# Kernel tuning notes

Hardware: AMD Instinct MI355X
Metric: run time of the kernel (lower is better)

Reference implementation:

```python
import jax, jax.numpy as jnp
import numpy as np

NUM_GRAPHS = 512

def setup_inputs() -> dict:
    key = jax.random.key(0)
    ks = jax.random.split(key, 16)
    N, E, F_IN, D = 50000, 800000, 128, 64
    x = jax.random.normal(ks[0], (N, F_IN), dtype=jnp.float32)
    edge_index = jax.random.randint(ks[1], (2, E), 0, N, dtype=jnp.int32)
    batch_index = jnp.sort(jax.random.randint(ks[2], (N,), 0, NUM_GRAPHS, dtype=jnp.int32))
    def lin(k, fin, fout):
        s = 1.0 / np.sqrt(fin)
        return jax.random.uniform(k, (fin, fout), jnp.float32, -s, s)
    return {
        "x": x, "edge_index": edge_index, "batch_index": batch_index,
        "W0": lin(ks[3], F_IN, D), "b0": jnp.zeros((D,), jnp.float32),
        "W1": lin(ks[4], D, D), "b1": jnp.zeros((D,), jnp.float32),
        "W2": lin(ks[5], D, D), "b2": jnp.zeros((D,), jnp.float32),
        "W3": lin(ks[6], D, D), "b3": jnp.zeros((D,), jnp.float32),
        "Wout": lin(ks[7], 2 * D, 1), "bout": jnp.zeros((1,), jnp.float32),
    }

def _gcn_edges(edge_index, N):
    # add self-loops and compute symmetric normalization D^-1/2 (A+I) D^-1/2
    loops = jnp.arange(N, dtype=edge_index.dtype)
    row = jnp.concatenate([edge_index[0], loops])  # source
    col = jnp.concatenate([edge_index[1], loops])  # target
    deg = jax.ops.segment_sum(jnp.ones_like(col, dtype=jnp.float32), col, num_segments=N)
    dinv = jnp.where(deg > 0, jax.lax.rsqrt(deg), 0.0)
    norm = dinv[row] * dinv[col]  # [E+N]
    return row, col, norm

def _gcn_conv(h, row, col, norm, W, b, N):
    h = h @ W                                   # [N, D] linear transform first
    msg = h[row] * norm[:, None]                # gather + scale
    out = jax.ops.segment_sum(msg, col, num_segments=N)  # scatter-add
    return out + b

def reference(x, edge_index, batch_index, W0, b0, W1, b1, W2, b2, W3, b3, Wout, bout):
    N = x.shape[0]
    row, col, norm = _gcn_edges(edge_index, N)
    h = jnp.tanh(_gcn_conv(x, row, col, norm, W0, b0, N))
    h = jnp.tanh(_gcn_conv(h, row, col, norm, W1, b1, N))
    h = jnp.tanh(_gcn_conv(h, row, col, norm, W2, b2, N))
    h = jnp.tanh(_gcn_conv(h, row, col, norm, W3, b3, N))
    gmax = jax.ops.segment_max(h, batch_index, num_segments=NUM_GRAPHS)
    gmax = jnp.where(jnp.isfinite(gmax), gmax, 0.0)  # empty segments -> 0
    gsum = jax.ops.segment_sum(h, batch_index, num_segments=NUM_GRAPHS)
    cnt = jax.ops.segment_sum(jnp.ones((N,), jnp.float32), batch_index, num_segments=NUM_GRAPHS)
    gmean = gsum / jnp.maximum(cnt, 1.0)[:, None]
    hidden = jnp.concatenate([gmax, gmean], axis=1)   # [G, 2D]
    out = hidden @ Wout + bout                        # [G, 1]
    return out, hidden
```

## Files before the change

kernel.cpp:

```cpp
#include <hip/hip_runtime.h>
#include <math.h>

#define CAP 64
typedef unsigned short ushort_t;
typedef unsigned int uint_t;

__global__ __launch_bounds__(256) void k_scatter2(const int* __restrict__ row,
                                                  const int* __restrict__ col, int E, int N,
                                                  int* __restrict__ deg, ushort_t* __restrict__ csr) {
    const int part = blockIdx.x & 7;
    const int slot = blockIdx.x >> 3;
    const int nslots = gridDim.x >> 3;
    const int lo = (int)((long long)N * part / 8);
    const int hi = (int)((long long)N * (part + 1) / 8);
    for (int e = slot * blockDim.x + threadIdx.x; e < E; e += nslots * blockDim.x) {
        int c = col[e];
        if (c >= lo && c < hi) {
            int d = atomicAdd(&deg[c], 1);
            if (d < CAP) csr[((size_t)c << 6) + d] = (ushort_t)row[e];
        }
    }
}

template <int K>
__global__ __launch_bounds__(256) void k_gemm(const float* __restrict__ X,
                                              const float* __restrict__ W,
                                              const int* __restrict__ deg,
                                              float* __restrict__ Gb, int N) {
    __shared__ __align__(16) float Wl[64 * 64];
    __shared__ __align__(16) float Xl[64 * 68];

    const int tid = threadIdx.x;
    const int wave = tid >> 6, lane = tid & 63;
    const int d8 = lane & 7, ns = lane >> 3;
    const int n0 = wave * 16 + ns, n1 = n0 + 8;

    const int base = blockIdx.x * 64;
    if (base >= N) return;
    const int tile_n = min(64, N - base);

    float4 a0l = {0,0,0,0}, a0h = {0,0,0,0}, a1l = {0,0,0,0}, a1h = {0,0,0,0};

    for (int kh = 0; kh < K / 64; kh++) {
        __syncthreads();
        for (int i = tid; i < 1024; i += 256)
            ((float4*)Wl)[i] = ((const float4*)(W + kh * 4096))[i];
        for (int idx = tid; idx < 1024; idx += 256) {
            int n = idx >> 4, q = idx & 15;
            float4 v = {0,0,0,0};
            if (n < tile_n) v = ((const float4*)(X + (size_t)(base + n) * K + kh * 64))[q];
            ((float4*)(Xl + n * 68))[q] = v;
        }
        __syncthreads();

        const float4* xq0 = (const float4*)(Xl + n0 * 68);
        const float4* xq1 = (const float4*)(Xl + n1 * 68);
        const float* wcol = Wl + d8 * 8;
#pragma unroll 2
        for (int kq = 0; kq < 16; kq++) {
            const float4 x4a = xq0[kq];
            const float4 x4b = xq1[kq];
            const float xs0[4] = {x4a.x, x4a.y, x4a.z, x4a.w};
            const float xs1[4] = {x4b.x, x4b.y, x4b.z, x4b.w};
#pragma unroll
            for (int j = 0; j < 4; j++) {
                const int k = kq * 4 + j;
                const float4 wa = *(const float4*)(wcol + k * 64);
                const float4 wb = *(const float4*)(wcol + k * 64 + 4);
                const float xa = xs0[j];
                const float xb = xs1[j];
                a0l.x = fmaf(xa, wa.x, a0l.x); a0l.y = fmaf(xa, wa.y, a0l.y);
                a0l.z = fmaf(xa, wa.z, a0l.z); a0l.w = fmaf(xa, wa.w, a0l.w);
                a0h.x = fmaf(xa, wb.x, a0h.x); a0h.y = fmaf(xa, wb.y, a0h.y);
                a0h.z = fmaf(xa, wb.z, a0h.z); a0h.w = fmaf(xa, wb.w, a0h.w);
                a1l.x = fmaf(xb, wa.x, a1l.x); a1l.y = fmaf(xb, wa.y, a1l.y);
                a1l.z = fmaf(xb, wa.z, a1l.z); a1l.w = fmaf(xb, wa.w, a1l.w);
                a1h.x = fmaf(xb, wb.x, a1h.x); a1h.y = fmaf(xb, wb.y, a1h.y);
                a1h.z = fmaf(xb, wb.z, a1h.z); a1h.w = fmaf(xb, wb.w, a1h.w);
            }
        }
    }

    int gn0 = base + n0, gn1 = base + n1;
    if (gn0 < N) {
        float s = rsqrtf((float)(deg[gn0] + 1));
        float4* ptr = (float4*)(Gb + (size_t)gn0 * 64);
        ptr[d8 * 2]     = make_float4(a0l.x * s, a0l.y * s, a0l.z * s, a0l.w * s);
        ptr[d8 * 2 + 1] = make_float4(a0h.x * s, a0h.y * s, a0h.z * s, a0h.w * s);
    }
    if (gn1 < N) {
        float s = rsqrtf((float)(deg[gn1] + 1));
        float4* ptr = (float4*)(Gb + (size_t)gn1 * 64);
        ptr[d8 * 2]     = make_float4(a1l.x * s, a1l.y * s, a1l.z * s, a1l.w * s);
        ptr[d8 * 2 + 1] = make_float4(a1h.x * s, a1h.y * s, a1h.z * s, a1h.w * s);
    }
}

__global__ __launch_bounds__(256) void k_agg(const float* __restrict__ Gb,
                                             const int* __restrict__ deg,
                                             const ushort_t* __restrict__ csr,
                                             const float* __restrict__ bias,
                                             float* __restrict__ H, int N) {
    int n = blockIdx.x * 4 + (threadIdx.x >> 6);
    if (n >= N) return;
    int lane = threadIdx.x & 63;
    int cnt = deg[n]; if (cnt > CAP) cnt = CAP;
    const ushort_t* rowp = csr + ((size_t)n << 6);
    float a0 = Gb[(size_t)n * 64 + lane];
    float a1 = 0.f, a2 = 0.f, a3 = 0.f, a4 = 0.f, a5 = 0.f, a6 = 0.f, a7 = 0.f;
    int i = 0;
    for (; i + 16 <= cnt; i += 16) {
        uint4 q0 = *(const uint4*)(rowp + i);
        uint4 q1 = *(const uint4*)(rowp + i + 8);
        int j0 = q0.x & 0xffff, j1 = q0.x >> 16, j2 = q0.y & 0xffff, j3 = q0.y >> 16;
        int j4 = q0.z & 0xffff, j5 = q0.z >> 16, j6 = q0.w & 0xffff, j7 = q0.w >> 16;
        int j8 = q1.x & 0xffff, j9 = q1.x >> 16, jA = q1.y & 0xffff, jB = q1.y >> 16;
        int jC = q1.z & 0xffff, jD = q1.z >> 16, jE = q1.w & 0xffff, jF = q1.w >> 16;
        float g0 = Gb[(size_t)j0 * 64 + lane], g1 = Gb[(size_t)j1 * 64 + lane];
        float g2 = Gb[(size_t)j2 * 64 + lane], g3 = Gb[(size_t)j3 * 64 + lane];
        float g4 = Gb[(size_t)j4 * 64 + lane], g5 = Gb[(size_t)j5 * 64 + lane];
        float g6 = Gb[(size_t)j6 * 64 + lane], g7 = Gb[(size_t)j7 * 64 + lane];
        float g8 = Gb[(size_t)j8 * 64 + lane], g9 = Gb[(size_t)j9 * 64 + lane];
        float gA = Gb[(size_t)jA * 64 + lane], gB = Gb[(size_t)jB * 64 + lane];
        float gC = Gb[(size_t)jC * 64 + lane], gD = Gb[(size_t)jD * 64 + lane];
        float gE = Gb[(size_t)jE * 64 + lane], gF = Gb[(size_t)jF * 64 + lane];
        a0 += g0; a1 += g1; a2 += g2; a3 += g3;
        a4 += g4; a5 += g5; a6 += g6; a7 += g7;
        a0 += g8; a1 += g9; a2 += gA; a3 += gB;
        a4 += gC; a5 += gD; a6 += gE; a7 += gF;
    }
    if (i + 8 <= cnt) {
        uint4 q = *(const uint4*)(rowp + i);
        int j0 = q.x & 0xffff, j1 = q.x >> 16, j2 = q.y & 0xffff, j3 = q.y >> 16;
        int j4 = q.z & 0xffff, j5 = q.z >> 16, j6 = q.w & 0xffff, j7 = q.w >> 16;
        a0 += Gb[(size_t)j0 * 64 + lane]; a1 += Gb[(size_t)j1 * 64 + lane];
        a2 += Gb[(size_t)j2 * 64 + lane]; a3 += Gb[(size_t)j3 * 64 + lane];
        a4 += Gb[(size_t)j4 * 64 + lane]; a5 += Gb[(size_t)j5 * 64 + lane];
        a6 += Gb[(size_t)j6 * 64 + lane]; a7 += Gb[(size_t)j7 * 64 + lane];
        i += 8;
    }
    if (i + 4 <= cnt) {
        uint2 q = *(const uint2*)(rowp + i);
        int j0 = q.x & 0xffff, j1 = q.x >> 16, j2 = q.y & 0xffff, j3 = q.y >> 16;
        a0 += Gb[(size_t)j0 * 64 + lane]; a1 += Gb[(size_t)j1 * 64 + lane];
        a2 += Gb[(size_t)j2 * 64 + lane]; a3 += Gb[(size_t)j3 * 64 + lane];
        i += 4;
    }
    if (i + 2 <= cnt) {
        uint_t q = *(const uint_t*)(rowp + i);
        a4 += Gb[(size_t)(q & 0xffff) * 64 + lane];
        a5 += Gb[(size_t)(q >> 16) * 64 + lane];
        i += 2;
    }
    if (i < cnt) a6 += Gb[(size_t)rowp[i] * 64 + lane];
    float acc = ((a0 + a1) + (a2 + a3)) + ((a4 + a5) + (a6 + a7));
    float dinv = rsqrtf((float)(cnt + 1));
    H[(size_t)n * 64 + lane] = tanhf(acc * dinv + bias[lane]);
}

__global__ __launch_bounds__(256) void k_pool(const float* __restrict__ H,
                                              const int* __restrict__ batch, int N, int Gn,
                                              const float* __restrict__ Wout,
                                              const float* __restrict__ bout,
                                              float* __restrict__ out,
                                              float* __restrict__ hidden) {
    int g = blockIdx.x * 4 + (threadIdx.x >> 6);
    if (g >= Gn) return;
    int lane = threadIdx.x & 63;
    int lo = 0, hi = N;
    while (lo < hi) { int m = (lo + hi) >> 1; if (batch[m] < g) lo = m + 1; else hi = m; }
    int s = lo;
    lo = s; hi = N;
    while (lo < hi) { int m = (lo + hi) >> 1; if (batch[m] < g + 1) lo = m + 1; else hi = m; }
    int c = lo - s;

    float m0 = -INFINITY, m1 = -INFINITY, m2 = -INFINITY, m3 = -INFINITY;
    float s0 = 0.f, s1 = 0.f, s2 = 0.f, s3 = 0.f;
    int n = s;
    for (; n + 3 < s + c; n += 4) {
        float v0 = H[(size_t)n * 64 + lane];
        float v1 = H[(size_t)(n + 1) * 64 + lane];
        float v2 = H[(size_t)(n + 2) * 64 + lane];
        float v3 = H[(size_t)(n + 3) * 64 + lane];
        m0 = fmaxf(m0, v0); s0 += v0;
        m1 = fmaxf(m1, v1); s1 += v1;
        m2 = fmaxf(m2, v2); s2 += v2;
        m3 = fmaxf(m3, v3); s3 += v3;
    }
    for (; n < s + c; n++) {
        float v = H[(size_t)n * 64 + lane];
        m0 = fmaxf(m0, v); s0 += v;
    }
    float vmax = fmaxf(fmaxf(m0, m1), fmaxf(m2, m3));
    float vsum = (s0 + s1) + (s2 + s3);
    float gmax = (c > 0) ? vmax : 0.f;
    float gmean = (c > 0) ? vsum / (float)c : 0.f;
    hidden[(size_t)g * 128 + lane] = gmax;
    hidden[(size_t)g * 128 + 64 + lane] = gmean;
    float p = fmaf(gmax, Wout[lane], gmean * Wout[64 + lane]);
    for (int o = 32; o > 0; o >>= 1) p += __shfl_down(p, o);
    if (lane == 0) out[g] = p + bout[0];
}

extern "C" void kernel_launch(void* const* d_in, const int* in_sizes, int n_in,
                              void* d_out, int out_size, void* d_ws, size_t ws_size,
                              hipStream_t stream) {
    const float* x    = (const float*)d_in[0];
    const int*   ei   = (const int*)d_in[1];
    const int*   batch= (const int*)d_in[2];
    const float* W0 = (const float*)d_in[3];  const float* b0 = (const float*)d_in[4];
    const float* W1 = (const float*)d_in[5];  const float* b1 = (const float*)d_in[6];
    const float* W2 = (const float*)d_in[7];  const float* b2 = (const float*)d_in[8];
    const float* W3 = (const float*)d_in[9];  const float* b3 = (const float*)d_in[10];
    const float* Wout = (const float*)d_in[11]; const float* bout = (const float*)d_in[12];

    const int N  = in_sizes[2];
    const int E  = in_sizes[1] / 2;
    const int Gn = out_size / 129;

    const int* row = ei;
    const int* col = ei + E;

    float* out_p    = (float*)d_out;
    float* hidden_p = out_p + Gn;

    char* wp = (char*)d_ws;
    auto alloc = [&](size_t bytes) { void* p = (void*)wp; wp += (bytes + 255) & ~(size_t)255; return p; };
    int*      deg  = (int*)alloc((size_t)N * 4);
    ushort_t* csr  = (ushort_t*)alloc((size_t)N * CAP * 2);
    float*    Gbuf = (float*)alloc((size_t)N * 64 * 4);
    float*    Ha   = (float*)alloc((size_t)N * 64 * 4);
    float*    Hb   = (float*)alloc((size_t)N * 64 * 4);

    hipMemsetAsync(deg, 0, (size_t)N * 4, stream);
    k_scatter2<<<2048, 256, 0, stream>>>(row, col, E, N, deg, csr);

    const int gblocks = (N + 63) / 64;
    const int ablocks = (N + 3) / 4;

    k_gemm<128><<<gblocks, 256, 0, stream>>>(x, W0, deg, Gbuf, N);
    k_agg<<<ablocks, 256, 0, stream>>>(Gbuf, deg, csr, b0, Ha, N);
    k_gemm<64><<<gblocks, 256, 0, stream>>>(Ha, W1, deg, Gbuf, N);
    k_agg<<<ablocks, 256, 0, stream>>>(Gbuf, deg, csr, b1, Hb, N);
    k_gemm<64><<<gblocks, 256, 0, stream>>>(Hb, W2, deg, Gbuf, N);
    k_agg<<<ablocks, 256, 0, stream>>>(Gbuf, deg, csr, b2, Ha, N);
    k_gemm<64><<<gblocks, 256, 0, stream>>>(Ha, W3, deg, Gbuf, N);
    k_agg<<<ablocks, 256, 0, stream>>>(Gbuf, deg, csr, b3, Hb, N);

    k_pool<<<(Gn + 3) / 4, 256, 0, stream>>>(Hb, batch, N, Gn, Wout, bout, out_p, hidden_p);
}
```

Measured before the change: 330.8 us.

## Fuse aggregation with next layer GEMM and final aggregation with pooling

Each layer's neighbor aggregation plus tanh now feeds directly into the next layer's 64x64 transform through shared memory, so each intermediate H is never written to or re-read from global memory. The last aggregation is merged into the graph pooling kernel, one block per graph, and the launch count falls from ten to six. The trade-offs are that each fused block runs the gather for 64 nodes serially per wave, 16 each, before its GEMM, and the pooling kernel gives only four waves to each graph's roughly 100 nodes. This could hurt latency hiding and load balance.

```diff
diff --git a/kernel.cpp b/kernel.cpp
--- a/kernel.cpp
+++ b/kernel.cpp
@@ -20,6 +20,59 @@
             if (d < CAP) csr[((size_t)c << 6) + d] = (ushort_t)row[e];
         }
     }
+}
+
+__device__ __forceinline__ float agg_gather(const float* __restrict__ Gb,
+                                            const ushort_t* __restrict__ rowp,
+                                            int cnt, int self, int lane) {
+    float a0 = Gb[(size_t)self * 64 + lane];
+    float a1 = 0.f, a2 = 0.f, a3 = 0.f, a4 = 0.f, a5 = 0.f, a6 = 0.f, a7 = 0.f;
+    int i = 0;
+    for (; i + 16 <= cnt; i += 16) {
+        uint4 q0 = *(const uint4*)(rowp + i);
+        uint4 q1 = *(const uint4*)(rowp + i + 8);
+        int j0 = q0.x & 0xffff, j1 = q0.x >> 16, j2 = q0.y & 0xffff, j3 = q0.y >> 16;
+        int j4 = q0.z & 0xffff, j5 = q0.z >> 16, j6 = q0.w & 0xffff, j7 = q0.w >> 16;
+        int j8 = q1.x & 0xffff, j9 = q1.x >> 16, jA = q1.y & 0xffff, jB = q1.y >> 16;
+        int jC = q1.z & 0xffff, jD = q1.z >> 16, jE = q1.w & 0xffff, jF = q1.w >> 16;
+        float g0 = Gb[(size_t)j0 * 64 + lane], g1 = Gb[(size_t)j1 * 64 + lane];
+        float g2 = Gb[(size_t)j2 * 64 + lane], g3 = Gb[(size_t)j3 * 64 + lane];
+        float g4 = Gb[(size_t)j4 * 64 + lane], g5 = Gb[(size_t)j5 * 64 + lane];
+        float g6 = Gb[(size_t)j6 * 64 + lane], g7 = Gb[(size_t)j7 * 64 + lane];
+        float g8 = Gb[(size_t)j8 * 64 + lane], g9 = Gb[(size_t)j9 * 64 + lane];
+        float gA = Gb[(size_t)jA * 64 + lane], gB = Gb[(size_t)jB * 64 + lane];
+        float gC = Gb[(size_t)jC * 64 + lane], gD = Gb[(size_t)jD * 64 + lane];
+        float gE = Gb[(size_t)jE * 64 + lane], gF = Gb[(size_t)jF * 64 + lane];
+        a0 += g0; a1 += g1; a2 += g2; a3 += g3;
+        a4 += g4; a5 += g5; a6 += g6; a7 += g7;
+        a0 += g8; a1 += g9; a2 += gA; a3 += gB;
+        a4 += gC; a5 += gD; a6 += gE; a7 += gF;
+    }
+    if (i + 8 <= cnt) {
+        uint4 q = *(const uint4*)(rowp + i);
+        int j0 = q.x & 0xffff, j1 = q.x >> 16, j2 = q.y & 0xffff, j3 = q.y >> 16;
+        int j4 = q.z & 0xffff, j5 = q.z >> 16, j6 = q.w & 0xffff, j7 = q.w >> 16;
+        a0 += Gb[(size_t)j0 * 64 + lane]; a1 += Gb[(size_t)j1 * 64 + lane];
+        a2 += Gb[(size_t)j2 * 64 + lane]; a3 += Gb[(size_t)j3 * 64 + lane];
+        a4 += Gb[(size_t)j4 * 64 + lane]; a5 += Gb[(size_t)j5 * 64 + lane];
+        a6 += Gb[(size_t)j6 * 64 + lane]; a7 += Gb[(size_t)j7 * 64 + lane];
+        i += 8;
+    }
+    if (i + 4 <= cnt) {
+        uint2 q = *(const uint2*)(rowp + i);
+        int j0 = q.x & 0xffff, j1 = q.x >> 16, j2 = q.y & 0xffff, j3 = q.y >> 16;
+        a0 += Gb[(size_t)j0 * 64 + lane]; a1 += Gb[(size_t)j1 * 64 + lane];
+        a2 += Gb[(size_t)j2 * 64 + lane]; a3 += Gb[(size_t)j3 * 64 + lane];
+        i += 4;
+    }
+    if (i + 2 <= cnt) {
+        uint_t q = *(const uint_t*)(rowp + i);
+        a4 += Gb[(size_t)(q & 0xffff) * 64 + lane];
+        a5 += Gb[(size_t)(q >> 16) * 64 + lane];
+        i += 2;
+    }
+    if (i < cnt) a6 += Gb[(size_t)rowp[i] * 64 + lane];
+    return ((a0 + a1) + (a2 + a3)) + ((a4 + a5) + (a6 + a7));
 }
 
 template <int K>
@@ -96,110 +149,126 @@
     }
 }
 
-__global__ __launch_bounds__(256) void k_agg(const float* __restrict__ Gb,
-                                             const int* __restrict__ deg,
-                                             const ushort_t* __restrict__ csr,
-                                             const float* __restrict__ bias,
-                                             float* __restrict__ H, int N) {
-    int n = blockIdx.x * 4 + (threadIdx.x >> 6);
-    if (n >= N) return;
-    int lane = threadIdx.x & 63;
-    int cnt = deg[n]; if (cnt > CAP) cnt = CAP;
-    const ushort_t* rowp = csr + ((size_t)n << 6);
-    float a0 = Gb[(size_t)n * 64 + lane];
-    float a1 = 0.f, a2 = 0.f, a3 = 0.f, a4 = 0.f, a5 = 0.f, a6 = 0.f, a7 = 0.f;
-    int i = 0;
-    for (; i + 16 <= cnt; i += 16) {
-        uint4 q0 = *(const uint4*)(rowp + i);
-        uint4 q1 = *(const uint4*)(rowp + i + 8);
-        int j0 = q0.x & 0xffff, j1 = q0.x >> 16, j2 = q0.y & 0xffff, j3 = q0.y >> 16;
-        int j4 = q0.z & 0xffff, j5 = q0.z >> 16, j6 = q0.w & 0xffff, j7 = q0.w >> 16;
-        int j8 = q1.x & 0xffff, j9 = q1.x >> 16, jA = q1.y & 0xffff, jB = q1.y >> 16;
-        int jC = q1.z & 0xffff, jD = q1.z >> 16, jE = q1.w & 0xffff, jF = q1.w >> 16;
-        float g0 = Gb[(size_t)j0 * 64 + lane], g1 = Gb[(size_t)j1 * 64 + lane];
-        float g2 = Gb[(size_t)j2 * 64 + lane], g3 = Gb[(size_t)j3 * 64 + lane];
-        float g4 = Gb[(size_t)j4 * 64 + lane], g5 = Gb[(size_t)j5 * 64 + lane];
-        float g6 = Gb[(size_t)j6 * 64 + lane], g7 = Gb[(size_t)j7 * 64 + lane];
-        float g8 = Gb[(size_t)j8 * 64 + lane], g9 = Gb[(size_t)j9 * 64 + lane];
-        float gA = Gb[(size_t)jA * 64 + lane], gB = Gb[(size_t)jB * 64 + lane];
-        float gC = Gb[(size_t)jC * 64 + lane], gD = Gb[(size_t)jD * 64 + lane];
-        float gE = Gb[(size_t)jE * 64 + lane], gF = Gb[(size_t)jF * 64 + lane];
-        a0 += g0; a1 += g1; a2 += g2; a3 += g3;
-        a4 += g4; a5 += g5; a6 += g6; a7 += g7;
-        a0 += g8; a1 += g9; a2 += gA; a3 += gB;
-        a4 += gC; a5 += gD; a6 += gE; a7 += gF;
-    }
-    if (i + 8 <= cnt) {
-        uint4 q = *(const uint4*)(rowp + i);
-        int j0 = q.x & 0xffff, j1 = q.x >> 16, j2 = q.y & 0xffff, j3 = q.y >> 16;
-        int j4 = q.z & 0xffff, j5 = q.z >> 16, j6 = q.w & 0xffff, j7 = q.w >> 16;
-        a0 += Gb[(size_t)j0 * 64 + lane]; a1 += Gb[(size_t)j1 * 64 + lane];
-        a2 += Gb[(size_t)j2 * 64 + lane]; a3 += Gb[(size_t)j3 * 64 + lane];
-        a4 += Gb[(size_t)j4 * 64 + lane]; a5 += Gb[(size_t)j5 * 64 + lane];
-        a6 += Gb[(size_t)j6 * 64 + lane]; a7 += Gb[(size_t)j7 * 64 + lane];
-        i += 8;
-    }
-    if (i + 4 <= cnt) {
-        uint2 q = *(const uint2*)(rowp + i);
-        int j0 = q.x & 0xffff, j1 = q.x >> 16, j2 = q.y & 0xffff, j3 = q.y >> 16;
-        a0 += Gb[(size_t)j0 * 64 + lane]; a1 += Gb[(size_t)j1 * 64 + lane];
-        a2 += Gb[(size_t)j2 * 64 + lane]; a3 += Gb[(size_t)j3 * 64 + lane];
-        i += 4;
-    }
-    if (i + 2 <= cnt) {
-        uint_t q = *(const uint_t*)(rowp + i);
-        a4 += Gb[(size_t)(q & 0xffff) * 64 + lane];
-        a5 += Gb[(size_t)(q >> 16) * 64 + lane];
-        i += 2;
-    }
-    if (i < cnt) a6 += Gb[(size_t)rowp[i] * 64 + lane];
-    float acc = ((a0 + a1) + (a2 + a3)) + ((a4 + a5) + (a6 + a7));
-    float dinv = rsqrtf((float)(cnt + 1));
-    H[(size_t)n * 64 + lane] = tanhf(acc * dinv + bias[lane]);
-}
-
-__global__ __launch_bounds__(256) void k_pool(const float* __restrict__ H,
-                                              const int* __restrict__ batch, int N, int Gn,
-                                              const float* __restrict__ Wout,
-                                              const float* __restrict__ bout,
-                                              float* __restrict__ out,
-                                              float* __restrict__ hidden) {
-    int g = blockIdx.x * 4 + (threadIdx.x >> 6);
-    if (g >= Gn) return;
-    int lane = threadIdx.x & 63;
+__global__ __launch_bounds__(256) void k_fused(const float* __restrict__ Gin,
+                                               const int* __restrict__ deg,
+                                               const ushort_t* __restrict__ csr,
+                                               const float* __restrict__ bias,
+                                               const float* __restrict__ W,
+                                               float* __restrict__ Gout, int N) {
+    __shared__ __align__(16) float Wl[64 * 64];
+    __shared__ __align__(16) float Hl[64 * 68];
+
+    const int tid = threadIdx.x;
+    const int wave = tid >> 6, lane = tid & 63;
+    const int base = blockIdx.x * 64;
+    if (base >= N) return;
+
+    for (int i = tid; i < 1024; i += 256) ((float4*)Wl)[i] = ((const float4*)W)[i];
+
+    const float bv = bias[lane];
+    for (int s = 0; s < 16; s++) {
+        const int ln = wave * 16 + s;
+        const int n = base + ln;
+        float val = 0.f;
+        if (n < N) {
+            int cnt = deg[n]; if (cnt > CAP) cnt = CAP;
+            float acc = agg_gather(Gin, csr + ((size_t)n << 6), cnt, n, lane);
+            val = tanhf(acc * rsqrtf((float)(cnt + 1)) + bv);
+        }
+        Hl[ln * 68 + lane] = val;
+    }
+    __syncthreads();
+
+    const int d8 = lane & 7, ns = lane >> 3;
+    const int n0 = wave * 16 + ns, n1 = n0 + 8;
+    const float4* xq0 = (const float4*)(Hl + n0 * 68);
+    const float4* xq1 = (const float4*)(Hl + n1 * 68);
+    const float* wcol = Wl + d8 * 8;
+    float4 a0l = {0,0,0,0}, a0h = {0,0,0,0}, a1l = {0,0,0,0}, a1h = {0,0,0,0};
+#pragma unroll 2
+    for (int kq = 0; kq < 16; kq++) {
+        const float4 x4a = xq0[kq];
+        const float4 x4b = xq1[kq];
+        const float xs0[4] = {x4a.x, x4a.y, x4a.z, x4a.w};
+        const float xs1[4] = {x4b.x, x4b.y, x4b.z, x4b.w};
+#pragma unroll
+        for (int j = 0; j < 4; j++) {
+            const int k = kq * 4 + j;
+            const float4 wa = *(const float4*)(wcol + k * 64);
+            const float4 wb = *(const float4*)(wcol + k * 64 + 4);
+            const float xa = xs0[j];
+            const float xb = xs1[j];
+            a0l.x = fmaf(xa, wa.x, a0l.x); a0l.y = fmaf(xa, wa.y, a0l.y);
+            a0l.z = fmaf(xa, wa.z, a0l.z); a0l.w = fmaf(xa, wa.w, a0l.w);
+            a0h.x = fmaf(xa, wb.x, a0h.x); a0h.y = fmaf(xa, wb.y, a0h.y);
+            a0h.z = fmaf(xa, wb.z, a0h.z); a0h.w = fmaf(xa, wb.w, a0h.w);
+            a1l.x = fmaf(xb, wa.x, a1l.x); a1l.y = fmaf(xb, wa.y, a1l.y);
+            a1l.z = fmaf(xb, wa.z, a1l.z); a1l.w = fmaf(xb, wa.w, a1l.w);
+            a1h.x = fmaf(xb, wb.x, a1h.x); a1h.y = fmaf(xb, wb.y, a1h.y);
+            a1h.z = fmaf(xb, wb.z, a1h.z); a1h.w = fmaf(xb, wb.w, a1h.w);
+        }
+    }
+
+    int gn0 = base + n0, gn1 = base + n1;
+    if (gn0 < N) {
+        float s = rsqrtf((float)(deg[gn0] + 1));
+        float4* ptr = (float4*)(Gout + (size_t)gn0 * 64);
+        ptr[d8 * 2]     = make_float4(a0l.x * s, a0l.y * s, a0l.z * s, a0l.w * s);
+        ptr[d8 * 2 + 1] = make_float4(a0h.x * s, a0h.y * s, a0h.z * s, a0h.w * s);
+    }
+    if (gn1 < N) {
+        float s = rsqrtf((float)(deg[gn1] + 1));
+        float4* ptr = (float4*)(Gout + (size_t)gn1 * 64);
+        ptr[d8 * 2]     = make_float4(a1l.x * s, a1l.y * s, a1l.z * s, a1l.w * s);
+        ptr[d8 * 2 + 1] = make_float4(a1h.x * s, a1h.y * s, a1h.z * s, a1h.w * s);
+    }
+}
+
+__global__ __launch_bounds__(256) void k_aggpool(const float* __restrict__ Gb,
+                                                 const int* __restrict__ deg,
+                                                 const ushort_t* __restrict__ csr,
+                                                 const int* __restrict__ batch, int N,
+                                                 const float* __restrict__ bias,
+                                                 const float* __restrict__ Wout,
+                                                 const float* __restrict__ bout,
+                                                 float* __restrict__ out,
+                                                 float* __restrict__ hidden) {
+    __shared__ float smax[4][64];
+    __shared__ float ssum[4][64];
+    const int g = blockIdx.x;
+    const int tid = threadIdx.x;
+    const int wave = tid >> 6, lane = tid & 63;
+
     int lo = 0, hi = N;
     while (lo < hi) { int m = (lo + hi) >> 1; if (batch[m] < g) lo = m + 1; else hi = m; }
-    int s = lo;
+    const int s = lo;
     lo = s; hi = N;
     while (lo < hi) { int m = (lo + hi) >> 1; if (batch[m] < g + 1) lo = m + 1; else hi = m; }
-    int c = lo - s;
-
-    float m0 = -INFINITY, m1 = -INFINITY, m2 = -INFINITY, m3 = -INFINITY;
-    float s0 = 0.f, s1 = 0.f, s2 = 0.f, s3 = 0.f;
-    int n = s;
-    for (; n + 3 < s + c; n += 4) {
-        float v0 = H[(size_t)n * 64 + lane];
-        float v1 = H[(size_t)(n + 1) * 64 + lane];
-        float v2 = H[(size_t)(n + 2) * 64 + lane];
-        float v3 = H[(size_t)(n + 3) * 64 + lane];
-        m0 = fmaxf(m0, v0); s0 += v0;
-        m1 = fmaxf(m1, v1); s1 += v1;
-        m2 = fmaxf(m2, v2); s2 += v2;
-        m3 = fmaxf(m3, v3); s3 += v3;
-    }
-    for (; n < s + c; n++) {
-        float v = H[(size_t)n * 64 + lane];
-        m0 = fmaxf(m0, v); s0 += v;
-    }
-    float vmax = fmaxf(fmaxf(m0, m1), fmaxf(m2, m3));
-    float vsum = (s0 + s1) + (s2 + s3);
-    float gmax = (c > 0) ? vmax : 0.f;
-    float gmean = (c > 0) ? vsum / (float)c : 0.f;
-    hidden[(size_t)g * 128 + lane] = gmax;
-    hidden[(size_t)g * 128 + 64 + lane] = gmean;
-    float p = fmaf(gmax, Wout[lane], gmean * Wout[64 + lane]);
-    for (int o = 32; o > 0; o >>= 1) p += __shfl_down(p, o);
-    if (lane == 0) out[g] = p + bout[0];
+    const int c = lo - s;
+
+    const float bv = bias[lane];
+    float vmax = -INFINITY, vsum = 0.f;
+    for (int n = s + wave; n < s + c; n += 4) {
+        int cnt = deg[n]; if (cnt > CAP) cnt = CAP;
+        float acc = agg_gather(Gb, csr + ((size_t)n << 6), cnt, n, lane);
+        float val = tanhf(acc * rsqrtf((float)(cnt + 1)) + bv);
+        vmax = fmaxf(vmax, val);
+        vsum += val;
+    }
+    smax[wave][lane] = vmax;
+    ssum[wave][lane] = vsum;
+    __syncthreads();
+    if (wave == 0) {
+        float m = fmaxf(fmaxf(smax[0][lane], smax[1][lane]), fmaxf(smax[2][lane], smax[3][lane]));
+        float su = (ssum[0][lane] + ssum[1][lane]) + (ssum[2][lane] + ssum[3][lane]);
+        float gmax = (c > 0) ? m : 0.f;
+        float gmean = (c > 0) ? su / (float)c : 0.f;
+        hidden[(size_t)g * 128 + lane] = gmax;
+        hidden[(size_t)g * 128 + 64 + lane] = gmean;
+        float p = fmaf(gmax, Wout[lane], gmean * Wout[64 + lane]);
+        for (int o = 32; o > 0; o >>= 1) p += __shfl_down(p, o);
+        if (lane == 0) out[g] = p + bout[0];
+    }
 }
 
 extern "C" void kernel_launch(void* const* d_in, const int* in_sizes, int n_in,
@@ -228,24 +297,17 @@
     auto alloc = [&](size_t bytes) { void* p = (void*)wp; wp += (bytes + 255) & ~(size_t)255; return p; };
     int*      deg  = (int*)alloc((size_t)N * 4);
     ushort_t* csr  = (ushort_t*)alloc((size_t)N * CAP * 2);
-    float*    Gbuf = (float*)alloc((size_t)N * 64 * 4);
-    float*    Ha   = (float*)alloc((size_t)N * 64 * 4);
-    float*    Hb   = (float*)alloc((size_t)N * 64 * 4);
+    float*    Ga   = (float*)alloc((size_t)N * 64 * 4);
+    float*    Gbx  = (float*)alloc((size_t)N * 64 * 4);
 
     hipMemsetAsync(deg, 0, (size_t)N * 4, stream);
     k_scatter2<<<2048, 256, 0, stream>>>(row, col, E, N, deg, csr);
 
     const int gblocks = (N + 63) / 64;
-    const int ablocks = (N + 3) / 4;
-
-    k_gemm<128><<<gblocks, 256, 0, stream>>>(x, W0, deg, Gbuf, N);
-    k_agg<<<ablocks, 256, 0, stream>>>(Gbuf, deg, csr, b0, Ha, N);
-    k_gemm<64><<<gblocks, 256, 0, stream>>>(Ha, W1, deg, Gbuf, N);
-    k_agg<<<ablocks, 256, 0, stream>>>(Gbuf, deg, csr, b1, Hb, N);
-    k_gemm<64><<<gblocks, 256, 0, stream>>>(Hb, W2, deg, Gbuf, N);
-    k_agg<<<ablocks, 256, 0, stream>>>(Gbuf, deg, csr, b2, Ha, N);
-    k_gemm<64><<<gblocks, 256, 0, stream>>>(Ha, W3, deg, Gbuf, N);
-    k_agg<<<ablocks, 256, 0, stream>>>(Gbuf, deg, csr, b3, Hb, N);
-
-    k_pool<<<(Gn + 3) / 4, 256, 0, stream>>>(Hb, batch, N, Gn, Wout, bout, out_p, hidden_p);
-}
+
+    k_gemm<128><<<gblocks, 256, 0, stream>>>(x, W0, deg, Ga, N);
+    k_fused<<<gblocks, 256, 0, stream>>>(Ga, deg, csr, b0, W1, Gbx, N);
+    k_fused<<<gblocks, 256, 0, stream>>>(Gbx, deg, csr, b1, W2, Ga, N);
+    k_fused<<<gblocks, 256, 0, stream>>>(Ga, deg, csr, b2, W3, Gbx, N);
+    k_aggpool<<<Gn, 256, 0, stream>>>(Gbx, deg, csr, batch, N, b3, Wout, bout, out_p, hidden_p);
+}
```

After: 365.8 us. 10.6% more time.
